# Performance work log

Hardware: AMD Instinct MI355X
Metric: run time of the kernel (lower is better)

Reference implementation:

```python
import jax, jax.numpy as jnp
import numpy as np

B, IMGS, PH, PW = 4, 4, 16, 16      # 4 groups, 4 images/group, 16x16 patches per image
P, C = 16, 3
N = IMGS * PH * PW                   # 1024 packed tokens per group
PATCH_DIM = C * P * P                # 768
DIM, HEADS, DHEAD, DEPTH = 768, 12, 64, 4
INNER = HEADS * DHEAD
MLP = 3072
POSMAX = 32                          # image_size // patch_size
NCLS = 1000
SCALE = DHEAD ** 0.5


def _ln(x, g):
    # torch LayerNorm with learned gamma, beta frozen at 0
    mu = jnp.mean(x, -1, keepdims=True)
    var = jnp.var(x, -1, keepdims=True)
    return (x - mu) * jax.lax.rsqrt(var + 1e-5) * g


def _qk_rmsnorm(t, g):
    # F.normalize(t, dim=-1) * sqrt(dhead) * gamma[h, 1, d]; t: (b,h,n,d), g: (h,d)
    nrm = jnp.sqrt(jnp.sum(t * t, -1, keepdims=True))
    return t / jnp.maximum(nrm, 1e-12) * SCALE * g[None, :, None, :]


def _attention(x, context, ln_g, Wq, Wkv, qg, kg, Wo, attn_mask):
    xn = _ln(x, ln_g)
    kv_in = xn if context is None else context  # context is NOT normed (matches torch)
    q = xn @ Wq
    k, v = jnp.split(kv_in @ Wkv, 2, axis=-1)
    split = lambda t: t.reshape(t.shape[0], t.shape[1], HEADS, DHEAD).transpose(0, 2, 1, 3)
    q, k, v = split(q), split(k), split(v)
    q = _qk_rmsnorm(q, qg)
    k = _qk_rmsnorm(k, kg)
    dots = jnp.einsum('bhid,bhjd->bhij', q, k)  # no 1/sqrt(d): scale lives in RMSNorm
    dots = jnp.where(attn_mask, dots, -jnp.finfo(dots.dtype).max)
    attn = jax.nn.softmax(dots, axis=-1)
    out = jnp.einsum('bhij,bhjd->bhid', attn, v)
    out = out.transpose(0, 2, 1, 3).reshape(x.shape[0], -1, INNER)
    return out @ Wo


def _forward(patches, emb_ln_g, W_emb, b_emb, emb_ln2_g, pos_h, pos_w,
             ln_attn_g, Wq, Wkv, qn_g, kn_g, Wo,
             ln_ff_g, W1, b1, W2, b2, final_ln_g,
             pool_q, pool_ln_g, pWq, pWkv, p_qn_g, p_kn_g, pWo,
             head_ln_g, W_head,
             patch_positions, image_ids, lengths):
    valid = jnp.arange(N)[None, :] < lengths[:, None]              # (B,N) True = real token
    same_img = image_ids[:, :, None] == image_ids[:, None, :]      # (B,i,j) block-diagonal
    attn_mask = (same_img & valid[:, None, :])[:, None]            # (B,1,i,j)

    x = _ln(patches, emb_ln_g) @ W_emb + b_emb
    x = _ln(x, emb_ln2_g)
    x = x + pos_h[patch_positions[..., 0]] + pos_w[patch_positions[..., 1]]

    for l in range(DEPTH):
        x = _attention(x, None, ln_attn_g[l], Wq[l], Wkv[l], qn_g[l], kn_g[l], Wo[l], attn_mask) + x
        h = jax.nn.gelu(_ln(x, ln_ff_g[l]) @ W1[l] + b1[l], approximate=False)
        x = h @ W2[l] + b2[l] + x
    x = _ln(x, final_ln_g)

    # attention pooling: one learned query per packed image
    queries = jnp.broadcast_to(pool_q, (x.shape[0], IMGS, DIM))
    pool_mask = ((jnp.arange(IMGS)[None, :, None] == image_ids[:, None, :]) & valid[:, None, :])[:, None]
    pooled = _attention(queries, x, pool_ln_g, pWq, pWkv, p_qn_g, p_kn_g, pWo, pool_mask) + queries
    return _ln(pooled, head_ln_g) @ W_head  # (B, IMGS, NCLS), mlp_head has no bias


def setup_inputs():
    key = jax.random.key(0)
    ks = jax.random.split(key, 20)
    rn = lambda k, shape, s=0.02: (jax.random.normal(k, shape) * s).astype(jnp.float32)

    patches = jax.random.normal(ks[0], (B, N, PATCH_DIM), dtype=jnp.float32)
    hh, ww = jnp.meshgrid(jnp.arange(PH), jnp.arange(PW), indexing='ij')
    pos = jnp.stack([hh.reshape(-1), ww.reshape(-1)], axis=-1)        # (256,2)
    patch_positions = jnp.broadcast_to(jnp.tile(pos, (IMGS, 1))[None], (B, N, 2)).astype(jnp.int32)
    image_ids = jnp.broadcast_to(jnp.repeat(jnp.arange(IMGS), PH * PW)[None], (B, N)).astype(jnp.int32)
    lengths = jnp.full((B,), N, dtype=jnp.int32)

    return dict(
        patches=patches, patch_positions=patch_positions, image_ids=image_ids, lengths=lengths,
        emb_ln_g=jnp.ones(PATCH_DIM, jnp.float32), W_emb=rn(ks[1], (PATCH_DIM, DIM)),
        b_emb=jnp.zeros(DIM, jnp.float32), emb_ln2_g=jnp.ones(DIM, jnp.float32),
        pos_h=rn(ks[2], (POSMAX, DIM), 1.0), pos_w=rn(ks[3], (POSMAX, DIM), 1.0),
        ln_attn_g=jnp.ones((DEPTH, DIM), jnp.float32),
        Wq=rn(ks[4], (DEPTH, DIM, INNER)), Wkv=rn(ks[5], (DEPTH, DIM, 2 * INNER)),
        qn_g=jnp.ones((DEPTH, HEADS, DHEAD), jnp.float32), kn_g=jnp.ones((DEPTH, HEADS, DHEAD), jnp.float32),
        Wo=rn(ks[6], (DEPTH, INNER, DIM)),
        ln_ff_g=jnp.ones((DEPTH, DIM), jnp.float32),
        W1=rn(ks[7], (DEPTH, DIM, MLP)), b1=jnp.zeros((DEPTH, MLP), jnp.float32),
        W2=rn(ks[8], (DEPTH, MLP, DIM)), b2=jnp.zeros((DEPTH, DIM), jnp.float32),
        final_ln_g=jnp.ones(DIM, jnp.float32),
        pool_q=rn(ks[9], (DIM,), 1.0), pool_ln_g=jnp.ones(DIM, jnp.float32),
        pWq=rn(ks[10], (DIM, INNER)), pWkv=rn(ks[11], (DIM, 2 * INNER)),
        p_qn_g=jnp.ones((HEADS, DHEAD), jnp.float32), p_kn_g=jnp.ones((HEADS, DHEAD), jnp.float32),
        pWo=rn(ks[12], (INNER, DIM)),
        head_ln_g=jnp.ones(DIM, jnp.float32), W_head=rn(ks[13], (DIM, NCLS)),
    )


def reference(patches, patch_positions, image_ids, lengths,
              emb_ln_g, W_emb, b_emb, emb_ln2_g, pos_h, pos_w,
              ln_attn_g, Wq, Wkv, qn_g, kn_g, Wo,
              ln_ff_g, W1, b1, W2, b2, final_ln_g,
              pool_q, pool_ln_g, pWq, pWkv, p_qn_g, p_kn_g, pWo,
              head_ln_g, W_head):
    return _forward(patches, emb_ln_g, W_emb, b_emb, emb_ln2_g, pos_h, pos_w,
                    ln_attn_g, Wq, Wkv, qn_g, kn_g, Wo,
                    ln_ff_g, W1, b1, W2, b2, final_ln_g,
                    pool_q, pool_ln_g, pWq, pWkv, p_qn_g, p_kn_g, pWo,
                    head_ln_g, W_head, patch_positions, image_ids, lengths)
```

## Files before the change

### kernel.cpp

```cpp
#include <hip/hip_runtime.h>
#include <hip/hip_bf16.h>
#include <math.h>

using bf16 = __hip_bfloat16;
typedef short s16x8 __attribute__((ext_vector_type(8)));
typedef float f32x4 __attribute__((ext_vector_type(4)));

#define DEVI __device__ __forceinline__

static constexpr int NB    = 4;
static constexpr int NTOK  = 1024;
static constexpr int DIM   = 768;
static constexpr int NH    = 12;
static constexpr int MLPD  = 3072;
static constexpr int NLAYER= 4;
static constexpr int NIMG  = 4;
static constexpr int NCLS  = 1000;
static constexpr int MR    = NB * NTOK;
static constexpr size_t SLAB = (size_t)MR * 768;

DEVI float b2f(bf16 v){ return __bfloat162float(v); }
DEVI bf16  f2b(float v){ return __float2bfloat16(v); }

DEVI void async16(const void* g, void* l) {
  __builtin_amdgcn_global_load_lds((const __attribute__((address_space(1))) void*)g,
                                   (__attribute__((address_space(3))) void*)l, 16, 0, 0);
}

DEVI f32x4 mfma16(s16x8 a, s16x8 b, f32x4 c) {
  return __builtin_amdgcn_mfma_f32_16x16x32_bf16(a, b, c, 0, 0, 0);
}

template<int N> DEVI void waitcnt_vm() {
  if constexpr (N == 0)      asm volatile("s_waitcnt vmcnt(0)" ::: "memory");
  else if constexpr (N == 3) asm volatile("s_waitcnt vmcnt(3)" ::: "memory");
  else if constexpr (N == 4) asm volatile("s_waitcnt vmcnt(4)" ::: "memory");
  else if constexpr (N == 6) asm volatile("s_waitcnt vmcnt(6)" ::: "memory");
}

DEVI float block_sum(float v, float* scratch, int tid) {
  #pragma unroll
  for (int o = 32; o >= 1; o >>= 1) v += __shfl_xor(v, o);
  __syncthreads();
  if ((tid & 63) == 0) scratch[tid >> 6] = v;
  __syncthreads();
  return scratch[0] + scratch[1] + scratch[2] + scratch[3];
}

DEVI float block_max(float v, float* scratch, int tid) {
  #pragma unroll
  for (int o = 32; o >= 1; o >>= 1) v = fmaxf(v, __shfl_xor(v, o));
  __syncthreads();
  if ((tid & 63) == 0) scratch[tid >> 6] = v;
  __syncthreads();
  return fmaxf(fmaxf(scratch[0], scratch[1]), fmaxf(scratch[2], scratch[3]));
}

struct bh4 { bf16 a, b, c, d; };
struct TEntry { const float* src; bf16* dst; int R, C, tiles, tC; };
struct TDesc  { TEntry e[22]; };

__global__ __launch_bounds__(256) void transpose_kernel(TDesc D, int nent) {
  int bid = blockIdx.x, ei = 0;
  while (ei < nent - 1 && bid >= D.e[ei].tiles) { bid -= D.e[ei].tiles; ++ei; }
  const TEntry E = D.e[ei];
  const int tr = bid / E.tC, tc = bid % E.tC;
  __shared__ bf16 t[32][33];
  const int tid = threadIdx.x;
  const int lr = tid >> 3, lc = (tid & 7) * 4;
  const float* srow = E.src + (size_t)(tr*32 + lr)*E.C + tc*32 + lc;
  float4 v = *(const float4*)srow;
  t[lr][lc] = f2b(v.x); t[lr][lc+1] = f2b(v.y); t[lr][lc+2] = f2b(v.z); t[lr][lc+3] = f2b(v.w);
  __syncthreads();
  bh4 o;
  o.a = t[lc+0][lr]; o.b = t[lc+1][lr]; o.c = t[lc+2][lr]; o.d = t[lc+3][lr];
  *(bh4*)(E.dst + (size_t)(tc*32 + lr)*E.R + tr*32 + lc) = o;
}

__global__ __launch_bounds__(256) void ln768_kernel(const float* __restrict__ in,
    const float* __restrict__ g, bf16* __restrict__ out)
{
  __shared__ float scratch[4];
  const int row = blockIdx.x, tid = threadIdx.x;
  const float* p = in + (size_t)row*768;
  const float v0 = p[tid], v1 = p[tid+256], v2 = p[tid+512];
  const float s  = block_sum(v0+v1+v2, scratch, tid);
  const float ss = block_sum(v0*v0+v1*v1+v2*v2, scratch, tid);
  const float mu = s * (1.0f/768.0f);
  const float var = ss * (1.0f/768.0f) - mu*mu;
  const float rstd = rsqrtf(var + 1e-5f);
  bf16* o = out + (size_t)row*768;
  o[tid]     = f2b((v0-mu)*rstd*g[tid]);
  o[tid+256] = f2b((v1-mu)*rstd*g[tid+256]);
  o[tid+512] = f2b((v2-mu)*rstd*g[tid+512]);
}

template<int HAS_BIAS>
__global__ __launch_bounds__(256) void res2_ln_kernel(float* __restrict__ x,
    const float* __restrict__ P, const float* __restrict__ bias,
    const float* __restrict__ g, bf16* __restrict__ xn)
{
  __shared__ float scratch[4];
  const int row = blockIdx.x, tid = threadIdx.x;
  const size_t base = (size_t)row*768;
  const float* p0 = P + base;
  const float* p1 = P + SLAB + base;
  float* xr = x + base;
  float v[3];
  #pragma unroll
  for (int i = 0; i < 3; ++i) {
    const int c = tid + i*256;
    float t = xr[c] + p0[c] + p1[c];
    if constexpr (HAS_BIAS) t += bias[c];
    v[i] = t;
    xr[c] = t;
  }
  const float s  = block_sum(v[0]+v[1]+v[2], scratch, tid);
  const float ss = block_sum(v[0]*v[0]+v[1]*v[1]+v[2]*v[2], scratch, tid);
  const float mu = s * (1.0f/768.0f);
  const float rstd = rsqrtf(ss*(1.0f/768.0f) - mu*mu + 1e-5f);
  bf16* o = xn + base;
  #pragma unroll
  for (int i = 0; i < 3; ++i) {
    const int c = tid + i*256;
    o[c] = f2b((v[i]-mu)*rstd*g[c]);
  }
}

__global__ __launch_bounds__(256) void ln_pos2_kernel(const float* __restrict__ P,
    const float* __restrict__ bias, const float* __restrict__ g,
    const float* __restrict__ pos_h, const float* __restrict__ pos_w,
    const int* __restrict__ ppos, float* __restrict__ out)
{
  __shared__ float scratch[4];
  const int row = blockIdx.x, tid = threadIdx.x;
  const size_t base = (size_t)row*768;
  const float* p0 = P + base;
  const float* p1 = P + SLAB + base;
  float v[3];
  #pragma unroll
  for (int i = 0; i < 3; ++i) {
    const int c = tid + i*256;
    v[i] = p0[c] + p1[c] + bias[c];
  }
  const float s  = block_sum(v[0]+v[1]+v[2], scratch, tid);
  const float ss = block_sum(v[0]*v[0]+v[1]*v[1]+v[2]*v[2], scratch, tid);
  const float mu = s * (1.0f/768.0f);
  const float rstd = rsqrtf(ss*(1.0f/768.0f) - mu*mu + 1e-5f);
  const int p0i = ppos[row*2], p1i = ppos[row*2+1];
  const float* ph = pos_h + (size_t)p0i*768;
  const float* pw = pos_w + (size_t)p1i*768;
  float* o = out + base;
  #pragma unroll
  for (int i = 0; i < 3; ++i) {
    const int c = tid + i*256;
    o[c] = (v[i]-mu)*rstd*g[c] + ph[c] + pw[c];
  }
}

template<int DO_BIAS, int DO_GELU, int OUT_BF16, int DO_RES, int NTILE, int SPLITK>
__global__ __launch_bounds__(256)
void gemm_mfma(const bf16* __restrict__ A, const bf16* __restrict__ BT,
               const float* __restrict__ bias, float* __restrict__ Cf,
               bf16* __restrict__ Cb, int M, int Nn, int K)
{
  constexpr int NF  = NTILE / 32;
  constexpr int PD  = 3;
  constexpr int LPI = 2 + NTILE/64;
  constexpr int VW  = (PD - 2) * LPI;
  __shared__ bf16 As[PD][64*64];
  __shared__ bf16 Bs[PD][(NTILE/2)*64];
  const int tid = threadIdx.x;
  const int wid = tid >> 6, lane = tid & 63;
  const int quad = lane >> 4, l15 = lane & 15;
  const int wy = wid >> 1, wx = wid & 1;

  const int gx  = gridDim.x;
  const int nwg = gx * gridDim.y;
  const int bid = blockIdx.y * gx + blockIdx.x;
  const int qq  = nwg >> 3, rm = nwg & 7;
  const int xcd = bid & 7,  li = bid >> 3;
  const int swz = (xcd < rm ? xcd * (qq + 1) : rm * (qq + 1) + (xcd - rm) * qq) + li;
  const int m0 = (swz / gx) * 128, n0 = (swz % gx) * NTILE;

  const int kz    = (SPLITK > 1) ? blockIdx.z : 0;
  const int kloc  = K / SPLITK;
  const int kbase = kz * kloc;

  const int rl = lane >> 3;
  const int cs = lane & 7;

  f32x4 acc[4][NF];
  #pragma unroll
  for (int i = 0; i < 4; ++i)
    #pragma unroll
    for (int j = 0; j < NF; ++j) acc[i][j] = (f32x4){0.f,0.f,0.f,0.f};

  auto stage = [&](int buf, int k0) {
    #pragma unroll
    for (int c = 0; c < 2; ++c) {
      const int rbase = wid*8 + c*32;
      const int r_abs = rbase + rl;
      const int ceff  = cs ^ (r_abs & 7);
      const int mg    = 2*r_abs + (ceff >> 2);
      const int jb    = (ceff & 3) * 16;
      async16((const char*)A + ((size_t)(m0 + mg)*K + k0)*2 + jb, (char*)As[buf] + rbase*128);
    }
    #pragma unroll
    for (int c = 0; c < NTILE/64; ++c) {
      const int rbase = wid*8 + c*32;
      const int r_abs = rbase + rl;
      const int ceff  = cs ^ (r_abs & 7);
      const int ng    = 2*r_abs + (ceff >> 2);
      const int jb    = (ceff & 3) * 16;
      async16((const char*)BT + ((size_t)(n0 + ng)*K + k0)*2 + jb, (char*)Bs[buf] + rbase*128);
    }
  };

  auto compute = [&](int cb) {
    s16x8 af[4], bfr[NF];
    #pragma unroll
    for (int mt = 0; mt < 4; ++mt) {
      const int m = wy*64 + mt*16 + l15;
      const int r = m >> 1;
      const int cq = (((m & 1) << 2) | quad) ^ (r & 7);
      af[mt] = *(const s16x8*)((const char*)As[cb] + r*128 + cq*16);
    }
    #pragma unroll
    for (int nt = 0; nt < NF; ++nt) {
      const int n = wx*(NTILE/2) + nt*16 + l15;
      const int r = n >> 1;
      const int cq = (((n & 1) << 2) | quad) ^ (r & 7);
      bfr[nt] = *(const s16x8*)((const char*)Bs[cb] + r*128 + cq*16);
    }
    #pragma unroll
    for (int mt = 0; mt < 4; ++mt)
      #pragma unroll
      for (int nt = 0; nt < NF; ++nt)
        acc[mt][nt] = mfma16(af[mt], bfr[nt], acc[mt][nt]);
  };

  const int nk = kloc >> 5;
  #pragma unroll
  for (int t = 0; t < PD - 1; ++t) stage(t, kbase + (t << 5));

  int cbuf = 0, sbuf = PD - 1;
  const int mainN = nk - (PD - 1);
  for (int kt = 0; kt < mainN; ++kt) {
    __builtin_amdgcn_sched_barrier(0);
    waitcnt_vm<VW>();
    __builtin_amdgcn_s_barrier();
    __builtin_amdgcn_sched_barrier(0);
    stage(sbuf, kbase + ((kt + PD - 1) << 5));
    compute(cbuf);
    cbuf = (cbuf + 1 == PD) ? 0 : cbuf + 1;
    sbuf = (sbuf + 1 == PD) ? 0 : sbuf + 1;
  }
  for (int kt = mainN; kt < nk; ++kt) {
    __builtin_amdgcn_sched_barrier(0);
    waitcnt_vm<0>();
    __builtin_amdgcn_s_barrier();
    __builtin_amdgcn_sched_barrier(0);
    compute(cbuf);
    cbuf = (cbuf + 1 == PD) ? 0 : cbuf + 1;
  }

  float* Cslab = (SPLITK > 1) ? (Cf + (size_t)kz * SLAB) : Cf;
  #pragma unroll
  for (int nt = 0; nt < NF; ++nt) {
    const int col = n0 + wx*(NTILE/2) + nt*16 + l15;
    float bv = 0.f;
    if constexpr (DO_BIAS) bv = bias[col];
    #pragma unroll
    for (int mt = 0; mt < 4; ++mt) {
      #pragma unroll
      for (int r = 0; r < 4; ++r) {
        const int row = m0 + wy*64 + mt*16 + quad*4 + r;
        float v = acc[mt][nt][r];
        if constexpr (DO_BIAS) v += bv;
        if constexpr (DO_GELU) v = 0.5f*v*(1.0f + erff(v*0.70710678118654752f));
        const size_t idx = (size_t)row*Nn + col;
        if constexpr (OUT_BF16) Cb[idx] = f2b(v);
        else if constexpr (DO_RES) Cslab[idx] += v;
        else Cslab[idx] = v;
      }
    }
  }
}

template<int IN_BF16, int DO_BIAS>
__global__ __launch_bounds__(256) void smallm_gemm(const void* __restrict__ Xv,
    const float* __restrict__ W, const float* __restrict__ bias,
    float* __restrict__ out, int Nn)
{
  __shared__ float Xs[16*768];
  __shared__ float red[4][16][64];
  const int tid = threadIdx.x;
  if constexpr (IN_BF16) {
    const bf16* X = (const bf16*)Xv;
    for (int i = tid; i < 16*768; i += 256) Xs[i] = b2f(X[i]);
  } else {
    const float* X = (const float*)Xv;
    for (int i = tid; i < 16*768; i += 256) Xs[i] = X[i];
  }
  __syncthreads();
  const int cl = tid & 63, kg = tid >> 6;
  const int c = blockIdx.x*64 + cl;
  float acc[16];
  #pragma unroll
  for (int r = 0; r < 16; ++r) acc[r] = 0.f;
  if (c < Nn) {
    const int k0 = kg*192;
    #pragma unroll 4
    for (int k = k0; k < k0 + 192; ++k) {
      const float w = W[(size_t)k*Nn + c];
      #pragma unroll
      for (int r = 0; r < 16; ++r) acc[r] += Xs[r*768 + k] * w;
    }
  }
  #pragma unroll
  for (int r = 0; r < 16; ++r) red[kg][r][cl] = acc[r];
  __syncthreads();
  if (kg == 0 && c < Nn) {
    #pragma unroll
    for (int r = 0; r < 16; ++r) {
      float v = red[0][r][cl] + red[1][r][cl] + red[2][r][cl] + red[3][r][cl];
      if constexpr (DO_BIAS) v += bias[c];
      out[(size_t)r*Nn + c] = v;
    }
  }
}

__global__ __launch_bounds__(256) void rms_qkv_kernel(const float* __restrict__ qkv,
    const float* __restrict__ qg, const float* __restrict__ kg,
    bf16* __restrict__ Qb, bf16* __restrict__ Kb, bf16* __restrict__ VTb)
{
  __shared__ float tile[64*68];
  const int nt = blockIdx.x, h = blockIdx.y, b = blockIdx.z;
  const int tid = threadIdx.x;
  const int bh = b*NH + h;
  const size_t rowbase = (size_t)(b*NTOK + nt*64);
  const int r = tid >> 2, pp = tid & 3;

  auto stage = [&](int off) {
    #pragma unroll
    for (int rr = 0; rr < 4; ++rr) {
      const int idx = rr*256 + tid;
      const int rw = idx >> 4, c4 = (idx & 15) << 2;
      float4 val = *(const float4*)(qkv + (rowbase + rw)*2304 + off + c4);
      *(float4*)(&tile[rw*68 + c4]) = val;
    }
  };

  stage(h*64);
  __syncthreads();
  {
    float ssq = 0.f;
    #pragma unroll
    for (int i = 0; i < 16; ++i) { float x = tile[r*68 + pp*16 + i]; ssq += x*x; }
    ssq += __shfl_xor(ssq, 1); ssq += __shfl_xor(ssq, 2);
    const float rn = 8.0f / fmaxf(sqrtf(ssq), 1e-12f);
    bf16* orow = Qb + ((size_t)bh*NTOK + nt*64 + r)*64;
    #pragma unroll
    for (int i = 0; i < 16; ++i) { int d = pp*16+i; orow[d] = f2b(tile[r*68+d]*rn*qg[h*64+d]); }
  }
  __syncthreads();
  stage(768 + h*64);
  __syncthreads();
  {
    float ssq = 0.f;
    #pragma unroll
    for (int i = 0; i < 16; ++i) { float x = tile[r*68 + pp*16 + i]; ssq += x*x; }
    ssq += __shfl_xor(ssq, 1); ssq += __shfl_xor(ssq, 2);
    const float rn = 8.0f / fmaxf(sqrtf(ssq), 1e-12f);
    bf16* orow = Kb + ((size_t)bh*NTOK + nt*64 + r)*64;
    #pragma unroll
    for (int i = 0; i < 16; ++i) { int d = pp*16+i; orow[d] = f2b(tile[r*68+d]*rn*kg[h*64+d]); }
  }
  __syncthreads();
  stage(1536 + h*64);
  __syncthreads();
  {
    const int d = tid >> 2;
    bf16* orow = VTb + ((size_t)bh*64 + d)*NTOK + nt*64;
    #pragma unroll
    for (int i = 0; i < 16; ++i) { int n = pp*16 + i; orow[n] = f2b(tile[n*68 + d]); }
  }
}

__global__ __launch_bounds__(256) void attn_mfma(const bf16* __restrict__ Qb,
    const bf16* __restrict__ Kb, const bf16* __restrict__ VTb, bf16* __restrict__ Ob,
    const int* __restrict__ ids, const int* __restrict__ lens)
{
  __shared__ bf16 Ps[4][16*72];
  __shared__ int  ids_s[NTOK];
  const int qt = blockIdx.x, h = blockIdx.y, b = blockIdx.z;
  const int tid = threadIdx.x;
  const int wid = tid >> 6, lane = tid & 63;
  const int quad = lane >> 4, l15 = lane & 15;
  const int bh = b*NH + h;
  const int q0 = qt*64;
  const int len = lens[b];

  #pragma unroll
  for (int i = 0; i < 4; ++i) ids_s[i*256 + tid] = ids[b*NTOK + i*256 + tid];
  __syncthreads();

  const bf16* qrow = Qb + ((size_t)bh*NTOK + q0 + wid*16 + l15)*64;
  const s16x8 aq0 = *(const s16x8*)(qrow + quad*8);
  const s16x8 aq1 = *(const s16x8*)(qrow + 32 + quad*8);

  int idq[4];
  #pragma unroll
  for (int rr = 0; rr < 4; ++rr) idq[rr] = ids_s[q0 + wid*16 + quad*4 + rr];

  unsigned qm = 0;
  #pragma unroll
  for (int rr = 0; rr < 4; ++rr) qm |= 1u << (idq[rr] & 31);
  #pragma unroll
  for (int o = 32; o >= 1; o >>= 1) qm |= (unsigned)__shfl_xor((int)qm, o);

  f32x4 oacc[4];
  #pragma unroll
  for (int nt = 0; nt < 4; ++nt) oacc[nt] = (f32x4){0.f,0.f,0.f,0.f};
  float mrow[4] = {-3.0e38f,-3.0e38f,-3.0e38f,-3.0e38f};
  float lrow[4] = {0.f,0.f,0.f,0.f};

  const bf16* Kgb = Kb  + (size_t)bh*NTOK*64;
  const bf16* Vgb = VTb + (size_t)bh*64*NTOK;
  bf16* pw = Ps[wid];

  for (int kt = 0; kt < 16; ++kt) {
    const int k0 = kt*64;
    const int idk_l = ids_s[k0 + lane];
    const bool ok = ((k0 + lane) < len) && (((qm >> (idk_l & 31)) & 1u) != 0u);
    if (__ballot(ok) == 0ULL) continue;

    f32x4 sA[4];
    #pragma unroll
    for (int jt = 0; jt < 4; ++jt) {
      const bf16* krow = Kgb + (size_t)(k0 + jt*16 + l15)*64;
      const s16x8 bk0 = *(const s16x8*)(krow + quad*8);
      const s16x8 bk1 = *(const s16x8*)(krow + 32 + quad*8);
      f32x4 s = (f32x4){0.f,0.f,0.f,0.f};
      s = mfma16(aq0, bk0, s);
      s = mfma16(aq1, bk1, s);
      sA[jt] = s;
    }
    #pragma unroll
    for (int jt = 0; jt < 4; ++jt) {
      const int j = k0 + jt*16 + l15;
      const int idk = ids_s[j];
      const bool kvld = j < len;
      #pragma unroll
      for (int rr = 0; rr < 4; ++rr)
        sA[jt][rr] = (kvld && idk == idq[rr]) ? sA[jt][rr] : -3.0e38f;
    }
    float alpha[4], mnew[4];
    #pragma unroll
    for (int rr = 0; rr < 4; ++rr) {
      float mx = fmaxf(fmaxf(sA[0][rr], sA[1][rr]), fmaxf(sA[2][rr], sA[3][rr]));
      mx = fmaxf(mx, __shfl_xor(mx, 1));
      mx = fmaxf(mx, __shfl_xor(mx, 2));
      mx = fmaxf(mx, __shfl_xor(mx, 4));
      mx = fmaxf(mx, __shfl_xor(mx, 8));
      const float mn = fmaxf(mrow[rr], mx);
      mnew[rr] = mn;
      alpha[rr] = expf(mrow[rr] - mn);
      mrow[rr] = mn;
    }
    #pragma unroll
    for (int rr = 0; rr < 4; ++rr) {
      float rs = 0.f;
      #pragma unroll
      for (int jt = 0; jt < 4; ++jt) {
        const float pv = (sA[jt][rr] > -1.0e38f) ? expf(sA[jt][rr] - mnew[rr]) : 0.0f;
        sA[jt][rr] = pv;
        rs += pv;
      }
      rs += __shfl_xor(rs, 1);
      rs += __shfl_xor(rs, 2);
      rs += __shfl_xor(rs, 4);
      rs += __shfl_xor(rs, 8);
      lrow[rr] = lrow[rr]*alpha[rr] + rs;
      #pragma unroll
      for (int nt = 0; nt < 4; ++nt) oacc[nt][rr] *= alpha[rr];
    }
    #pragma unroll
    for (int jt = 0; jt < 4; ++jt)
      #pragma unroll
      for (int rr = 0; rr < 4; ++rr)
        pw[(quad*4+rr)*72 + jt*16 + l15] = f2b(sA[jt][rr]);
    #pragma unroll
    for (int ss = 0; ss < 2; ++ss) {
      const s16x8 ap = *(const s16x8*)(pw + l15*72 + ss*32 + quad*8);
      #pragma unroll
      for (int nt = 0; nt < 4; ++nt) {
        const s16x8 bv = *(const s16x8*)(Vgb + (size_t)(nt*16 + l15)*NTOK + k0 + ss*32 + quad*8);
        oacc[nt] = mfma16(ap, bv, oacc[nt]);
      }
    }
  }

  #pragma unroll
  for (int rr = 0; rr < 4; ++rr) {
    const float inv = lrow[rr] > 0.f ? 1.0f/lrow[rr] : 0.0f;
    const int n = q0 + wid*16 + quad*4 + rr;
    bf16* orow = Ob + ((size_t)b*NTOK + n)*768 + h*64;
    #pragma unroll
    for (int nt = 0; nt < 4; ++nt)
      orow[nt*16 + l15] = f2b(oacc[nt][rr]*inv);
  }
}

__global__ __launch_bounds__(256) void pool_q_kernel(const float* __restrict__ pool_q,
    const float* __restrict__ pool_ln_g, const float* __restrict__ pWq,
    const float* __restrict__ p_qn_g, float* __restrict__ qp)
{
  __shared__ float xn[768];
  __shared__ float scratch[4];
  __shared__ float qraw[64];
  const int h = blockIdx.x, tid = threadIdx.x;
  float v0 = pool_q[tid], v1 = pool_q[tid+256], v2 = pool_q[tid+512];
  const float s  = block_sum(v0+v1+v2, scratch, tid);
  const float ss = block_sum(v0*v0+v1*v1+v2*v2, scratch, tid);
  const float mu = s*(1.0f/768.0f);
  const float rstd = rsqrtf(ss*(1.0f/768.0f) - mu*mu + 1e-5f);
  xn[tid]     = (v0-mu)*rstd*pool_ln_g[tid];
  xn[tid+256] = (v1-mu)*rstd*pool_ln_g[tid+256];
  xn[tid+512] = (v2-mu)*rstd*pool_ln_g[tid+512];
  __syncthreads();
  const int d = tid >> 2, pp = tid & 3;
  const int col = h*64 + d;
  float acc = 0.f;
  for (int k = pp*192; k < (pp+1)*192; ++k) acc += xn[k]*pWq[(size_t)k*768 + col];
  acc += __shfl_xor(acc, 1); acc += __shfl_xor(acc, 2);
  if (pp == 0) qraw[d] = acc;
  __syncthreads();
  if (tid < 64) {
    const float q = qraw[tid];
    float sq = q*q;
    #pragma unroll
    for (int o = 32; o >= 1; o >>= 1) sq += __shfl_xor(sq, o);
    const float rn = 8.0f / fmaxf(sqrtf(sq), 1e-12f);
    qp[h*64 + tid] = q * rn * p_qn_g[h*64 + tid];
  }
}

__global__ __launch_bounds__(256) void pool_attn_kernel(const float* __restrict__ kvp,
    const float* __restrict__ qp, const float* __restrict__ kg,
    const int* __restrict__ ids, const int* __restrict__ lens, float* __restrict__ pooled)
{
  __shared__ float sp[1024];
  __shared__ float qg_s[64];
  __shared__ float scratch[4];
  __shared__ float outred[4][64];
  const int h = blockIdx.x, img = blockIdx.y, b = blockIdx.z;
  const int tid = threadIdx.x;
  const int len = lens[b];
  if (tid < 64) qg_s[tid] = qp[h*64 + tid] * kg[h*64 + tid];
  __syncthreads();

  float smax = -3.0e38f;
  for (int j = tid; j < 1024; j += 256) {
    float sv = -3.0e38f;
    if (j < len && ids[b*NTOK + j] == img) {
      const float* kr = kvp + (size_t)(b*NTOK + j)*1536 + h*64;
      float ssq = 0.f, dq = 0.f;
      #pragma unroll
      for (int dd = 0; dd < 64; dd += 4) {
        float4 k4 = *(const float4*)(kr + dd);
        ssq += k4.x*k4.x + k4.y*k4.y + k4.z*k4.z + k4.w*k4.w;
        dq  += qg_s[dd]*k4.x + qg_s[dd+1]*k4.y + qg_s[dd+2]*k4.z + qg_s[dd+3]*k4.w;
      }
      const float rn = 8.0f / fmaxf(sqrtf(ssq), 1e-12f);
      sv = dq * rn;
    }
    sp[j] = sv;
    smax = fmaxf(smax, sv);
  }
  const float M = block_max(smax, scratch, tid);
  float lsum = 0.f;
  for (int j = tid; j < 1024; j += 256) {
    const float p = (sp[j] > -1.0e38f) ? expf(sp[j] - M) : 0.0f;
    sp[j] = p;
    lsum += p;
  }
  const float L = block_sum(lsum, scratch, tid);
  const float invL = L > 0.f ? 1.0f / L : 0.0f;

  const int d = tid & 63, jg = tid >> 6;
  float acc = 0.f;
  for (int j = jg; j < 1024; j += 4) {
    const float p = sp[j];
    if (p > 0.f) acc += p * kvp[(size_t)(b*NTOK + j)*1536 + 768 + h*64 + d];
  }
  outred[jg][d] = acc;
  __syncthreads();
  if (tid < 64) {
    const float o = (outred[0][tid] + outred[1][tid] + outred[2][tid] + outred[3][tid]) * invL;
    pooled[((size_t)b*NIMG + img)*768 + h*64 + tid] = o;
  }
}

extern "C" void kernel_launch(void* const* d_in, const int* in_sizes, int n_in,
                              void* d_out, int out_size, void* d_ws, size_t ws_size,
                              hipStream_t stream)
{
  const float* patches    = (const float*)d_in[0];
  const int*   ppos       = (const int*)d_in[1];
  const int*   image_ids  = (const int*)d_in[2];
  const int*   lengths    = (const int*)d_in[3];
  const float* emb_ln_g   = (const float*)d_in[4];
  const float* W_emb      = (const float*)d_in[5];
  const float* b_emb      = (const float*)d_in[6];
  const float* emb_ln2_g  = (const float*)d_in[7];
  const float* pos_h      = (const float*)d_in[8];
  const float* pos_w      = (const float*)d_in[9];
  const float* ln_attn_g  = (const float*)d_in[10];
  const float* Wq         = (const float*)d_in[11];
  const float* Wkv        = (const float*)d_in[12];
  const float* qn_g       = (const float*)d_in[13];
  const float* kn_g       = (const float*)d_in[14];
  const float* Wo         = (const float*)d_in[15];
  const float* ln_ff_g    = (const float*)d_in[16];
  const float* W1         = (const float*)d_in[17];
  const float* b1         = (const float*)d_in[18];
  const float* W2         = (const float*)d_in[19];
  const float* b2v        = (const float*)d_in[20];
  const float* final_ln_g = (const float*)d_in[21];
  const float* pool_q     = (const float*)d_in[22];
  const float* pool_ln_g  = (const float*)d_in[23];
  const float* pWq        = (const float*)d_in[24];
  const float* pWkv       = (const float*)d_in[25];
  const float* p_qn_g     = (const float*)d_in[26];
  const float* p_kn_g     = (const float*)d_in[27];
  const float* pWo        = (const float*)d_in[28];
  const float* head_ln_g  = (const float*)d_in[29];
  const float* W_head     = (const float*)d_in[30];

  char* ws = (char*)d_ws;
  size_t off = 0;
  auto alloc = [&](size_t sz){ size_t r = off; off += (sz + 255) & ~(size_t)255; return r; };

  const size_t o_WembT = alloc((size_t)768*768*2);
  size_t o_QKVT[4], o_WoT[4], o_W1T[4], o_W2T[4];
  for (int l = 0; l < NLAYER; ++l) {
    o_QKVT[l] = alloc((size_t)2304*768*2);
    o_WoT[l]  = alloc((size_t)768*768*2);
    o_W1T[l]  = alloc((size_t)3072*768*2);
    o_W2T[l]  = alloc((size_t)768*3072*2);
  }
  const size_t o_pWkvT = alloc((size_t)1536*768*2);
  const size_t o_x     = alloc((size_t)MR*768*4);
  const size_t o_xn    = alloc((size_t)MR*768*2);
  const size_t o_qkv   = alloc((size_t)MR*2304*4);
  const size_t o_P     = alloc((size_t)2*SLAB*4);
  const size_t o_Qb    = alloc((size_t)MR*768*2);
  const size_t o_Kb    = alloc((size_t)MR*768*2);
  const size_t o_VT    = alloc((size_t)MR*768*2);
  const size_t o_Ob    = alloc((size_t)MR*768*2);
  const size_t o_qp    = alloc((size_t)768*4);
  const size_t o_pool  = alloc((size_t)16*768*4);
  const size_t o_poolf = alloc((size_t)16*768*4);
  const size_t o_hl    = alloc((size_t)16*768*2);
  if (off > ws_size) return;

  float* x    = (float*)(ws + o_x);
  bf16*  xn   = (bf16*)(ws + o_xn);
  float* qkv  = (float*)(ws + o_qkv);
  bf16*  hb   = (bf16*)(ws + o_qkv);
  float* P    = (float*)(ws + o_P);
  bf16*  Qb   = (bf16*)(ws + o_Qb);
  bf16*  Kb   = (bf16*)(ws + o_Kb);
  bf16*  VTb  = (bf16*)(ws + o_VT);
  bf16*  Ob   = (bf16*)(ws + o_Ob);
  float* qp   = (float*)(ws + o_qp);
  float* pooled  = (float*)(ws + o_pool);
  float* pooledf = (float*)(ws + o_poolf);
  bf16*  hl   = (bf16*)(ws + o_hl);

  TDesc td; int ne = 0, total = 0;
  auto add = [&](const float* s, size_t dofs, int R, int C){
    td.e[ne].src = s;
    td.e[ne].dst = (bf16*)(ws + dofs);
    td.e[ne].R = R; td.e[ne].C = C;
    td.e[ne].tiles = (R/32)*(C/32); td.e[ne].tC = C/32;
    total += td.e[ne].tiles; ++ne;
  };
  add(W_emb, o_WembT, 768, 768);
  for (int l = 0; l < NLAYER; ++l) {
    add(Wq  + (size_t)l*768*768,  o_QKVT[l],                 768, 768);
    add(Wkv + (size_t)l*768*1536, o_QKVT[l] + (size_t)768*768*2, 768, 1536);
    add(Wo  + (size_t)l*768*768,  o_WoT[l],                  768, 768);
    add(W1  + (size_t)l*768*3072, o_W1T[l],                  768, 3072);
    add(W2  + (size_t)l*3072*768, o_W2T[l],                  3072, 768);
  }
  add(pWkv, o_pWkvT, 768, 1536);
  transpose_kernel<<<total, 256, 0, stream>>>(td, ne);

  ln768_kernel<<<MR, 256, 0, stream>>>(patches, emb_ln_g, xn);
  gemm_mfma<0,0,0,0,64,2><<<dim3(12,32,2), 256, 0, stream>>>(xn, (const bf16*)(ws+o_WembT), nullptr,
                                                             P, nullptr, MR, 768, 768);
  ln_pos2_kernel<<<MR, 256, 0, stream>>>(P, b_emb, emb_ln2_g, pos_h, pos_w, ppos, x);
  ln768_kernel<<<MR, 256, 0, stream>>>(x, ln_attn_g, xn);

  for (int l = 0; l < NLAYER; ++l) {
    gemm_mfma<0,0,0,0,64,1><<<dim3(36,32), 256, 0, stream>>>(xn, (const bf16*)(ws+o_QKVT[l]), nullptr,
                                                             qkv, nullptr, MR, 2304, 768);
    rms_qkv_kernel<<<dim3(16,NH,NB), 256, 0, stream>>>(qkv, qn_g + (size_t)l*768, kn_g + (size_t)l*768,
                                                       Qb, Kb, VTb);
    attn_mfma<<<dim3(16,NH,NB), 256, 0, stream>>>(Qb, Kb, VTb, Ob, image_ids, lengths);
    gemm_mfma<0,0,0,0,64,2><<<dim3(12,32,2), 256, 0, stream>>>(Ob, (const bf16*)(ws+o_WoT[l]), nullptr,
                                                               P, nullptr, MR, 768, 768);
    res2_ln_kernel<0><<<MR, 256, 0, stream>>>(x, P, nullptr, ln_ff_g + (size_t)l*768, xn);
    gemm_mfma<1,1,1,0,128,1><<<dim3(24,32), 256, 0, stream>>>(xn, (const bf16*)(ws+o_W1T[l]), b1 + (size_t)l*3072,
                                                              nullptr, hb, MR, 3072, 768);
    gemm_mfma<0,0,0,0,64,2><<<dim3(12,32,2), 256, 0, stream>>>(hb, (const bf16*)(ws+o_W2T[l]), nullptr,
                                                               P, nullptr, MR, 768, 3072);
    const float* gnext = (l + 1 < NLAYER) ? (ln_attn_g + (size_t)(l+1)*768) : final_ln_g;
    res2_ln_kernel<1><<<MR, 256, 0, stream>>>(x, P, b2v + (size_t)l*768, gnext, xn);
  }

  gemm_mfma<0,0,0,0,64,1><<<dim3(24,32), 256, 0, stream>>>(xn, (const bf16*)(ws+o_pWkvT), nullptr,
                                                           qkv, nullptr, MR, 1536, 768);
  pool_q_kernel<<<NH, 256, 0, stream>>>(pool_q, pool_ln_g, pWq, p_qn_g, qp);
  pool_attn_kernel<<<dim3(NH,NIMG,NB), 256, 0, stream>>>(qkv, qp, p_kn_g, image_ids, lengths, pooled);
  smallm_gemm<0,1><<<12, 256, 0, stream>>>(pooled, pWo, pool_q, pooledf, 768);
  ln768_kernel<<<16, 256, 0, stream>>>(pooledf, head_ln_g, hl);
  smallm_gemm<1,0><<<16, 256, 0, stream>>>(hl, W_head, nullptr, (float*)d_out, NCLS);
}
```

Before: 1.122 ms.

## Fuse QK RMSNorm and V transpose into QKV GEMM epilogue, plus LN fusion

The QKV projection GEMM now does the per-head RMSNorm of Q and K and the transposed V write in its epilogue, using a shared-memory reduction across the two wave columns. This removes the fp32 qkv round trip and the separate rms_qkv kernel. The embedding LN+pos kernel also computes the first attention LayerNorm, and the pooling KV GEMM writes bf16 instead of fp32. The weight transpose kernel now uses 64x64 tiles with 16-byte stores. The costs are extra epilogue work, an added barrier, and bf16 rounding of the pooling K/V before normalization.

```diff
diff --git a/kernel.cpp b/kernel.cpp
--- a/kernel.cpp
+++ b/kernel.cpp
@@ -4,6 +4,7 @@
 
 using bf16 = __hip_bfloat16;
 typedef short s16x8 __attribute__((ext_vector_type(8)));
+typedef short s16x4 __attribute__((ext_vector_type(4)));
 typedef float f32x4 __attribute__((ext_vector_type(4)));
 
 #define DEVI __device__ __forceinline__
@@ -21,6 +22,8 @@
 
 DEVI float b2f(bf16 v){ return __bfloat162float(v); }
 DEVI bf16  f2b(float v){ return __float2bfloat16(v); }
+DEVI float bu2f(unsigned short u){ union{unsigned u32; float f;} w; w.u32 = ((unsigned)u)<<16; return w.f; }
+DEVI unsigned short f2bu(float f){ bf16 b = f2b(f); return *(unsigned short*)&b; }
 
 DEVI void async16(const void* g, void* l) {
   __builtin_amdgcn_global_load_lds((const __attribute__((address_space(1))) void*)g,
@@ -56,7 +59,6 @@
   return fmaxf(fmaxf(scratch[0], scratch[1]), fmaxf(scratch[2], scratch[3]));
 }
 
-struct bh4 { bf16 a, b, c, d; };
 struct TEntry { const float* src; bf16* dst; int R, C, tiles, tC; };
 struct TDesc  { TEntry e[22]; };
 
@@ -65,16 +67,30 @@
   while (ei < nent - 1 && bid >= D.e[ei].tiles) { bid -= D.e[ei].tiles; ++ei; }
   const TEntry E = D.e[ei];
   const int tr = bid / E.tC, tc = bid % E.tC;
-  __shared__ bf16 t[32][33];
+  __shared__ unsigned short t[64][68];
   const int tid = threadIdx.x;
-  const int lr = tid >> 3, lc = (tid & 7) * 4;
-  const float* srow = E.src + (size_t)(tr*32 + lr)*E.C + tc*32 + lc;
-  float4 v = *(const float4*)srow;
-  t[lr][lc] = f2b(v.x); t[lr][lc+1] = f2b(v.y); t[lr][lc+2] = f2b(v.z); t[lr][lc+3] = f2b(v.w);
-  __syncthreads();
-  bh4 o;
-  o.a = t[lc+0][lr]; o.b = t[lc+1][lr]; o.c = t[lc+2][lr]; o.d = t[lc+3][lr];
-  *(bh4*)(E.dst + (size_t)(tc*32 + lr)*E.R + tr*32 + lc) = o;
+  {
+    const int r = tid >> 4, c = (tid & 15) * 4;
+    float4 v[4];
+    #pragma unroll
+    for (int p = 0; p < 4; ++p)
+      v[p] = *(const float4*)(E.src + (size_t)(tr*64 + p*16 + r)*E.C + tc*64 + c);
+    #pragma unroll
+    for (int p = 0; p < 4; ++p) {
+      unsigned short* dst = &t[p*16 + r][c];
+      dst[0] = f2bu(v[p].x); dst[1] = f2bu(v[p].y); dst[2] = f2bu(v[p].z); dst[3] = f2bu(v[p].w);
+    }
+  }
+  __syncthreads();
+  #pragma unroll
+  for (int p = 0; p < 2; ++p) {
+    const int n = p*32 + (tid >> 3);
+    const int r0 = (tid & 7) * 8;
+    s16x8 o;
+    #pragma unroll
+    for (int i = 0; i < 8; ++i) o[i] = (short)t[r0 + i][n];
+    *(s16x8*)((short*)E.dst + (size_t)(tc*64 + n)*E.R + tr*64 + r0) = o;
+  }
 }
 
 __global__ __launch_bounds__(256) void ln768_kernel(const float* __restrict__ in,
@@ -130,7 +146,8 @@
 __global__ __launch_bounds__(256) void ln_pos2_kernel(const float* __restrict__ P,
     const float* __restrict__ bias, const float* __restrict__ g,
     const float* __restrict__ pos_h, const float* __restrict__ pos_w,
-    const int* __restrict__ ppos, float* __restrict__ out)
+    const int* __restrict__ ppos, float* __restrict__ out,
+    const float* __restrict__ g2, bf16* __restrict__ xn)
 {
   __shared__ float scratch[4];
   const int row = blockIdx.x, tid = threadIdx.x;
@@ -151,18 +168,33 @@
   const float* ph = pos_h + (size_t)p0i*768;
   const float* pw = pos_w + (size_t)p1i*768;
   float* o = out + base;
+  float xv[3];
   #pragma unroll
   for (int i = 0; i < 3; ++i) {
     const int c = tid + i*256;
-    o[c] = (v[i]-mu)*rstd*g[c] + ph[c] + pw[c];
-  }
-}
-
-template<int DO_BIAS, int DO_GELU, int OUT_BF16, int DO_RES, int NTILE, int SPLITK>
+    xv[i] = (v[i]-mu)*rstd*g[c] + ph[c] + pw[c];
+    o[c] = xv[i];
+  }
+  const float s2  = block_sum(xv[0]+xv[1]+xv[2], scratch, tid);
+  const float ss2 = block_sum(xv[0]*xv[0]+xv[1]*xv[1]+xv[2]*xv[2], scratch, tid);
+  const float mu2 = s2 * (1.0f/768.0f);
+  const float rstd2 = rsqrtf(ss2*(1.0f/768.0f) - mu2*mu2 + 1e-5f);
+  bf16* on = xn + base;
+  #pragma unroll
+  for (int i = 0; i < 3; ++i) {
+    const int c = tid + i*256;
+    on[c] = f2b((xv[i]-mu2)*rstd2*g2[c]);
+  }
+}
+
+template<int DO_BIAS, int DO_GELU, int OUT_BF16, int DO_RES, int NTILE, int SPLITK, int RMSQKV>
 __global__ __launch_bounds__(256)
 void gemm_mfma(const bf16* __restrict__ A, const bf16* __restrict__ BT,
                const float* __restrict__ bias, float* __restrict__ Cf,
-               bf16* __restrict__ Cb, int M, int Nn, int K)
+               bf16* __restrict__ Cb,
+               const float* __restrict__ qg, const float* __restrict__ kg,
+               bf16* __restrict__ Qp, bf16* __restrict__ Kp, bf16* __restrict__ Vp,
+               int M, int Nn, int K)
 {
   constexpr int NF  = NTILE / 32;
   constexpr int PD  = 3;
@@ -265,24 +297,83 @@
     cbuf = (cbuf + 1 == PD) ? 0 : cbuf + 1;
   }
 
-  float* Cslab = (SPLITK > 1) ? (Cf + (size_t)kz * SLAB) : Cf;
-  #pragma unroll
-  for (int nt = 0; nt < NF; ++nt) {
-    const int col = n0 + wx*(NTILE/2) + nt*16 + l15;
-    float bv = 0.f;
-    if constexpr (DO_BIAS) bv = bias[col];
-    #pragma unroll
-    for (int mt = 0; mt < 4; ++mt) {
-      #pragma unroll
-      for (int r = 0; r < 4; ++r) {
-        const int row = m0 + wy*64 + mt*16 + quad*4 + r;
-        float v = acc[mt][nt][r];
-        if constexpr (DO_BIAS) v += bv;
-        if constexpr (DO_GELU) v = 0.5f*v*(1.0f + erff(v*0.70710678118654752f));
-        const size_t idx = (size_t)row*Nn + col;
-        if constexpr (OUT_BF16) Cb[idx] = f2b(v);
-        else if constexpr (DO_RES) Cslab[idx] += v;
-        else Cslab[idx] = v;
+  if constexpr (RMSQKV) {
+    __shared__ float red[128][2];
+    const int hg = n0 >> 6;
+    const int region = hg / NH;
+    const int h  = hg - region*NH;
+    const int b  = m0 >> 10;
+    const int bh = b*NH + h;
+    const int tokb = m0 & (NTOK-1);
+    if (region < 2) {
+      float sl[4][4];
+      #pragma unroll
+      for (int mt = 0; mt < 4; ++mt)
+        #pragma unroll
+        for (int rr = 0; rr < 4; ++rr) {
+          float ssq = 0.f;
+          #pragma unroll
+          for (int nt = 0; nt < NF; ++nt) ssq += acc[mt][nt][rr]*acc[mt][nt][rr];
+          #pragma unroll
+          for (int o = 1; o <= 8; o <<= 1) ssq += __shfl_xor(ssq, o);
+          sl[mt][rr] = ssq;
+        }
+      if (l15 == 0) {
+        #pragma unroll
+        for (int mt = 0; mt < 4; ++mt)
+          #pragma unroll
+          for (int rr = 0; rr < 4; ++rr)
+            red[wy*64 + mt*16 + quad*4 + rr][wx] = sl[mt][rr];
+      }
+      __syncthreads();
+      const float* gp = (region == 0) ? (qg + n0) : (kg + (n0 - 768));
+      bf16* outb = (region == 0) ? Qp : Kp;
+      #pragma unroll
+      for (int mt = 0; mt < 4; ++mt)
+        #pragma unroll
+        for (int rr = 0; rr < 4; ++rr) {
+          const int rlc = wy*64 + mt*16 + quad*4 + rr;
+          const float rn = 8.0f / fmaxf(sqrtf(red[rlc][0] + red[rlc][1]), 1e-12f);
+          const int tok = tokb + rlc;
+          #pragma unroll
+          for (int nt = 0; nt < NF; ++nt) {
+            const int d = wx*32 + nt*16 + l15;
+            outb[((size_t)bh*NTOK + tok)*64 + d] = f2b(acc[mt][nt][rr]*rn*gp[d]);
+          }
+        }
+    } else {
+      #pragma unroll
+      for (int mt = 0; mt < 4; ++mt)
+        #pragma unroll
+        for (int nt = 0; nt < NF; ++nt) {
+          const int d = wx*32 + nt*16 + l15;
+          const int tok = tokb + wy*64 + mt*16 + quad*4;
+          s16x4 pk;
+          #pragma unroll
+          for (int rr = 0; rr < 4; ++rr) pk[rr] = (short)f2bu(acc[mt][nt][rr]);
+          *(s16x4*)((short*)Vp + ((size_t)bh*64 + d)*NTOK + tok) = pk;
+        }
+    }
+  } else {
+    float* Cslab = (SPLITK > 1) ? (Cf + (size_t)kz * SLAB) : Cf;
+    #pragma unroll
+    for (int nt = 0; nt < NF; ++nt) {
+      const int col = n0 + wx*(NTILE/2) + nt*16 + l15;
+      float bv = 0.f;
+      if constexpr (DO_BIAS) bv = bias[col];
+      #pragma unroll
+      for (int mt = 0; mt < 4; ++mt) {
+        #pragma unroll
+        for (int r = 0; r < 4; ++r) {
+          const int row = m0 + wy*64 + mt*16 + quad*4 + r;
+          float v = acc[mt][nt][r];
+          if constexpr (DO_BIAS) v += bv;
+          if constexpr (DO_GELU) v = 0.5f*v*(1.0f + erff(v*0.70710678118654752f));
+          const size_t idx = (size_t)row*Nn + col;
+          if constexpr (OUT_BF16) Cb[idx] = f2b(v);
+          else if constexpr (DO_RES) Cslab[idx] += v;
+          else Cslab[idx] = v;
+        }
       }
     }
   }
@@ -328,63 +419,6 @@
       if constexpr (DO_BIAS) v += bias[c];
       out[(size_t)r*Nn + c] = v;
     }
-  }
-}
-
-__global__ __launch_bounds__(256) void rms_qkv_kernel(const float* __restrict__ qkv,
-    const float* __restrict__ qg, const float* __restrict__ kg,
-    bf16* __restrict__ Qb, bf16* __restrict__ Kb, bf16* __restrict__ VTb)
-{
-  __shared__ float tile[64*68];
-  const int nt = blockIdx.x, h = blockIdx.y, b = blockIdx.z;
-  const int tid = threadIdx.x;
-  const int bh = b*NH + h;
-  const size_t rowbase = (size_t)(b*NTOK + nt*64);
-  const int r = tid >> 2, pp = tid & 3;
-
-  auto stage = [&](int off) {
-    #pragma unroll
-    for (int rr = 0; rr < 4; ++rr) {
-      const int idx = rr*256 + tid;
-      const int rw = idx >> 4, c4 = (idx & 15) << 2;
-      float4 val = *(const float4*)(qkv + (rowbase + rw)*2304 + off + c4);
-      *(float4*)(&tile[rw*68 + c4]) = val;
-    }
-  };
-
-  stage(h*64);
-  __syncthreads();
-  {
-    float ssq = 0.f;
-    #pragma unroll
-    for (int i = 0; i < 16; ++i) { float x = tile[r*68 + pp*16 + i]; ssq += x*x; }
-    ssq += __shfl_xor(ssq, 1); ssq += __shfl_xor(ssq, 2);
-    const float rn = 8.0f / fmaxf(sqrtf(ssq), 1e-12f);
-    bf16* orow = Qb + ((size_t)bh*NTOK + nt*64 + r)*64;
-    #pragma unroll
-    for (int i = 0; i < 16; ++i) { int d = pp*16+i; orow[d] = f2b(tile[r*68+d]*rn*qg[h*64+d]); }
-  }
-  __syncthreads();
-  stage(768 + h*64);
-  __syncthreads();
-  {
-    float ssq = 0.f;
-    #pragma unroll
-    for (int i = 0; i < 16; ++i) { float x = tile[r*68 + pp*16 + i]; ssq += x*x; }
-    ssq += __shfl_xor(ssq, 1); ssq += __shfl_xor(ssq, 2);
-    const float rn = 8.0f / fmaxf(sqrtf(ssq), 1e-12f);
-    bf16* orow = Kb + ((size_t)bh*NTOK + nt*64 + r)*64;
-    #pragma unroll
-    for (int i = 0; i < 16; ++i) { int d = pp*16+i; orow[d] = f2b(tile[r*68+d]*rn*kg[h*64+d]); }
-  }
-  __syncthreads();
-  stage(1536 + h*64);
-  __syncthreads();
-  {
-    const int d = tid >> 2;
-    bf16* orow = VTb + ((size_t)bh*64 + d)*NTOK + nt*64;
-    #pragma unroll
-    for (int i = 0; i < 16; ++i) { int n = pp*16 + i; orow[n] = f2b(tile[n*68 + d]); }
   }
 }
 
@@ -547,7 +581,7 @@
   }
 }
 
-__global__ __launch_bounds__(256) void pool_attn_kernel(const float* __restrict__ kvp,
+__global__ __launch_bounds__(256) void pool_attn_kernel(const bf16* __restrict__ kvp,
     const float* __restrict__ qp, const float* __restrict__ kg,
     const int* __restrict__ ids, const int* __restrict__ lens, float* __restrict__ pooled)
 {
@@ -565,13 +599,17 @@
   for (int j = tid; j < 1024; j += 256) {
     float sv = -3.0e38f;
     if (j < len && ids[b*NTOK + j] == img) {
-      const float* kr = kvp + (size_t)(b*NTOK + j)*1536 + h*64;
+      const bf16* kr = kvp + (size_t)(b*NTOK + j)*1536 + h*64;
       float ssq = 0.f, dq = 0.f;
       #pragma unroll
-      for (int dd = 0; dd < 64; dd += 4) {
-        float4 k4 = *(const float4*)(kr + dd);
-        ssq += k4.x*k4.x + k4.y*k4.y + k4.z*k4.z + k4.w*k4.w;
-        dq  += qg_s[dd]*k4.x + qg_s[dd+1]*k4.y + qg_s[dd+2]*k4.z + qg_s[dd+3]*k4.w;
+      for (int dd = 0; dd < 64; dd += 8) {
+        s16x8 k8 = *(const s16x8*)(kr + dd);
+        #pragma unroll
+        for (int i = 0; i < 8; ++i) {
+          const float kv = bu2f((unsigned short)k8[i]);
+          ssq += kv*kv;
+          dq  += qg_s[dd+i]*kv;
+        }
       }
       const float rn = 8.0f / fmaxf(sqrtf(ssq), 1e-12f);
       sv = dq * rn;
@@ -593,7 +631,7 @@
   float acc = 0.f;
   for (int j = jg; j < 1024; j += 4) {
     const float p = sp[j];
-    if (p > 0.f) acc += p * kvp[(size_t)(b*NTOK + j)*1536 + 768 + h*64 + d];
+    if (p > 0.f) acc += p * b2f(kvp[(size_t)(b*NTOK + j)*1536 + 768 + h*64 + d]);
   }
   outred[jg][d] = acc;
   __syncthreads();
@@ -654,7 +692,7 @@
   const size_t o_pWkvT = alloc((size_t)1536*768*2);
   const size_t o_x     = alloc((size_t)MR*768*4);
   const size_t o_xn    = alloc((size_t)MR*768*2);
-  const size_t o_qkv   = alloc((size_t)MR*2304*4);
+  const size_t o_kv    = alloc((size_t)MR*3072*2);
   const size_t o_P     = alloc((size_t)2*SLAB*4);
   const size_t o_Qb    = alloc((size_t)MR*768*2);
   const size_t o_Kb    = alloc((size_t)MR*768*2);
@@ -668,8 +706,8 @@
 
   float* x    = (float*)(ws + o_x);
   bf16*  xn   = (bf16*)(ws + o_xn);
-  float* qkv  = (float*)(ws + o_qkv);
-  bf16*  hb   = (bf16*)(ws + o_qkv);
+  bf16*  hb   = (bf16*)(ws + o_kv);
+  bf16*  kvb  = (bf16*)(ws + o_kv);
   float* P    = (float*)(ws + o_P);
   bf16*  Qb   = (bf16*)(ws + o_Qb);
   bf16*  Kb   = (bf16*)(ws + o_Kb);
@@ -685,7 +723,7 @@
     td.e[ne].src = s;
     td.e[ne].dst = (bf16*)(ws + dofs);
     td.e[ne].R = R; td.e[ne].C = C;
-    td.e[ne].tiles = (R/32)*(C/32); td.e[ne].tC = C/32;
+    td.e[ne].tiles = (R/64)*(C/64); td.e[ne].tC = C/64;
     total += td.e[ne].tiles; ++ne;
   };
   add(W_emb, o_WembT, 768, 768);
@@ -700,32 +738,29 @@
   transpose_kernel<<<total, 256, 0, stream>>>(td, ne);
 
   ln768_kernel<<<MR, 256, 0, stream>>>(patches, emb_ln_g, xn);
-  gemm_mfma<0,0,0,0,64,2><<<dim3(12,32,2), 256, 0, stream>>>(xn, (const bf16*)(ws+o_WembT), nullptr,
-                                                             P, nullptr, MR, 768, 768);
-  ln_pos2_kernel<<<MR, 256, 0, stream>>>(P, b_emb, emb_ln2_g, pos_h, pos_w, ppos, x);
-  ln768_kernel<<<MR, 256, 0, stream>>>(x, ln_attn_g, xn);
+  gemm_mfma<0,0,0,0,64,2,0><<<dim3(12,32,2), 256, 0, stream>>>(xn, (const bf16*)(ws+o_WembT), nullptr,
+      P, nullptr, nullptr, nullptr, nullptr, nullptr, nullptr, MR, 768, 768);
+  ln_pos2_kernel<<<MR, 256, 0, stream>>>(P, b_emb, emb_ln2_g, pos_h, pos_w, ppos, x, ln_attn_g, xn);
 
   for (int l = 0; l < NLAYER; ++l) {
-    gemm_mfma<0,0,0,0,64,1><<<dim3(36,32), 256, 0, stream>>>(xn, (const bf16*)(ws+o_QKVT[l]), nullptr,
-                                                             qkv, nullptr, MR, 2304, 768);
-    rms_qkv_kernel<<<dim3(16,NH,NB), 256, 0, stream>>>(qkv, qn_g + (size_t)l*768, kn_g + (size_t)l*768,
-                                                       Qb, Kb, VTb);
+    gemm_mfma<0,0,0,0,64,1,1><<<dim3(36,32), 256, 0, stream>>>(xn, (const bf16*)(ws+o_QKVT[l]), nullptr,
+        nullptr, nullptr, qn_g + (size_t)l*768, kn_g + (size_t)l*768, Qb, Kb, VTb, MR, 2304, 768);
     attn_mfma<<<dim3(16,NH,NB), 256, 0, stream>>>(Qb, Kb, VTb, Ob, image_ids, lengths);
-    gemm_mfma<0,0,0,0,64,2><<<dim3(12,32,2), 256, 0, stream>>>(Ob, (const bf16*)(ws+o_WoT[l]), nullptr,
-                                                               P, nullptr, MR, 768, 768);
+    gemm_mfma<0,0,0,0,64,2,0><<<dim3(12,32,2), 256, 0, stream>>>(Ob, (const bf16*)(ws+o_WoT[l]), nullptr,
+        P, nullptr, nullptr, nullptr, nullptr, nullptr, nullptr, MR, 768, 768);
     res2_ln_kernel<0><<<MR, 256, 0, stream>>>(x, P, nullptr, ln_ff_g + (size_t)l*768, xn);
-    gemm_mfma<1,1,1,0,128,1><<<dim3(24,32), 256, 0, stream>>>(xn, (const bf16*)(ws+o_W1T[l]), b1 + (size_t)l*3072,
-                                                              nullptr, hb, MR, 3072, 768);
-    gemm_mfma<0,0,0,0,64,2><<<dim3(12,32,2), 256, 0, stream>>>(hb, (const bf16*)(ws+o_W2T[l]), nullptr,
-                                                               P, nullptr, MR, 768, 3072);
+    gemm_mfma<1,1,1,0,128,1,0><<<dim3(24,32), 256, 0, stream>>>(xn, (const bf16*)(ws+o_W1T[l]), b1 + (size_t)l*3072,
+        nullptr, hb, nullptr, nullptr, nullptr, nullptr, nullptr, MR, 3072, 768);
+    gemm_mfma<0,0,0,0,64,2,0><<<dim3(12,32,2), 256, 0, stream>>>(hb, (const bf16*)(ws+o_W2T[l]), nullptr,
+        P, nullptr, nullptr, nullptr, nullptr, nullptr, nullptr, MR, 768, 3072);
     const float* gnext = (l + 1 < NLAYER) ? (ln_attn_g + (size_t)(l+1)*768) : final_ln_g;
     res2_ln_kernel<1><<<MR, 256, 0, stream>>>(x, P, b2v + (size_t)l*768, gnext, xn);
   }
 
-  gemm_mfma<0,0,0,0,64,1><<<dim3(24,32), 256, 0, stream>>>(xn, (const bf16*)(ws+o_pWkvT), nullptr,
-                                                           qkv, nullptr, MR, 1536, 768);
+  gemm_mfma<0,0,1,0,64,1,0><<<dim3(24,32), 256, 0, stream>>>(xn, (const bf16*)(ws+o_pWkvT), nullptr,
+      nullptr, kvb, nullptr, nullptr, nullptr, nullptr, nullptr, MR, 1536, 768);
   pool_q_kernel<<<NH, 256, 0, stream>>>(pool_q, pool_ln_g, pWq, p_qn_g, qp);
-  pool_attn_kernel<<<dim3(NH,NIMG,NB), 256, 0, stream>>>(qkv, qp, p_kn_g, image_ids, lengths, pooled);
+  pool_attn_kernel<<<dim3(NH,NIMG,NB), 256, 0, stream>>>(kvb, qp, p_kn_g, image_ids, lengths, pooled);
   smallm_gemm<0,1><<<12, 256, 0, stream>>>(pooled, pWo, pool_q, pooledf, 768);
   ln768_kernel<<<16, 256, 0, stream>>>(pooledf, head_ln_g, hl);
   smallm_gemm<1,0><<<16, 256, 0, stream>>>(hl, W_head, nullptr, (float*)d_out, NCLS);
```

Result: faster. 1.089 ms (-3.0%).
